# Kernel tuning notes

Hardware: AMD Instinct MI355X
Metric: run time of the kernel (lower is better)

The kernel has to match this reference:

```python
import jax, jax.numpy as jnp
import numpy as np

# --- configuration (matches init_kwargs) ---
K = 8            # number of cluster fields
L = 8            # hashgrid levels
T = 2 ** 18      # hash table size per level (log2_hashmap_size=18)
F = 2            # features per level
HID = 64         # MLP hidden dim
BASE_RES = 16    # base resolution; max_res=2048 -> growth factor 2
N_PTS = 524288

PRIMES = np.array([1, 2654435761, 805459861], dtype=np.uint32)
RES = (BASE_RES * 2 ** np.arange(L)).astype(np.float32)  # [16,32,...,2048]
CORNERS = np.array([[i, j, k] for i in (0, 1) for j in (0, 1) for k in (0, 1)],
                   dtype=np.float32)  # [8,3] trilinear corner offsets


def setup_inputs() -> dict:
    key = jax.random.key(0)
    ks = jax.random.split(key, 6)
    return {
        "positions": jax.random.uniform(ks[0], (N_PTS, 3), dtype=jnp.float32),
        "centroids": jax.random.uniform(ks[1], (K, 3), dtype=jnp.float32),
        "tables":    jax.random.normal(ks[2], (K, L, T, F), dtype=jnp.float32) * 1e-2,
        "W1":        jax.random.normal(ks[3], (K, L * F, HID), dtype=jnp.float32) * 0.1,
        "b1":        jnp.zeros((K, HID), dtype=jnp.float32),
        "W2":        jax.random.normal(ks[4], (K, HID, 1), dtype=jnp.float32) * 0.1,
        "b2":        jnp.zeros((K, 1), dtype=jnp.float32),
    }


def _hash_encode(positions, tables, assign):
    """Multi-resolution hash encoding, table selected per-point by cluster assignment."""
    N = positions.shape[0]
    res = jnp.asarray(RES)                                    # [L]
    scaled = positions[:, None, :] * res[None, :, None]       # [N,L,3]
    f = jnp.floor(scaled)
    w = scaled - f                                            # [N,L,3] trilinear fracs
    corners = jnp.asarray(CORNERS)                            # [8,3]
    ci = (f[:, :, None, :] + corners[None, None]).astype(jnp.uint32)  # [N,L,8,3]
    p = jnp.asarray(PRIMES)
    h = (ci[..., 0] * p[0]) ^ (ci[..., 1] * p[1]) ^ (ci[..., 2] * p[2])
    h = (h & jnp.uint32(T - 1)).astype(jnp.int32)             # [N,L,8]
    lvl = jnp.arange(L, dtype=jnp.int32)
    # flat index into [K*L*T, F] table selects the assigned field's grid
    flat = (assign[:, None, None] * L + lvl[None, :, None]) * T + h   # [N,L,8]
    feats = tables.reshape(K * L * T, F)[flat]                # [N,L,8,F] gather
    cw = jnp.prod(jnp.where(corners[None, None] > 0.5,
                            w[:, :, None, :], 1.0 - w[:, :, None, :]), axis=-1)  # [N,L,8]
    enc = jnp.sum(feats * cw[..., None], axis=2)              # [N,L,F]
    return enc.reshape(N, L * F)


def reference(positions, centroids, tables, W1, b1, W2, b2):
    # cdist + argmin cluster routing
    d2 = jnp.sum((positions[:, None, :] - centroids[None]) ** 2, axis=-1)  # [N,K]
    assign = jnp.argmin(d2, axis=1).astype(jnp.int32)                      # [N]
    enc = _hash_encode(positions, tables, assign)                          # [N, L*F]
    dens = jnp.zeros((positions.shape[0], 1), dtype=positions.dtype)
    for k in range(K):  # small fixed loop over structurally distinct fields
        h = jax.nn.relu(enc @ W1[k] + b1[k])
        dk = jnp.exp(h @ W2[k] + b2[k])  # trunc_exp density activation
        dens = jnp.where((assign == k)[:, None], dk, dens)
    return dens  # [N,1]
```

## Files before the change

kernel.cpp:

```cpp
#include <hip/hip_runtime.h>
#include <hip/hip_fp16.h>
#include <math.h>

#define KF 8
#define LL 8
#define TT (1 << 18)
#define FF 2
#define HID 64
#define INF 16
#define W1S 1056
#define BS  68

#define NENT (KF * LL * TT)
#define TAB_BYTES ((size_t)NENT * 4)


__global__ __launch_bounds__(256) void repack_tables_fp16(
    const float4* __restrict__ src, uint4* __restrict__ dst, int nthreads)
{
    const int gid = blockIdx.x * blockDim.x + threadIdx.x;
    if (gid >= nthreads) return;
    const size_t b = (size_t)gid * 4;

    const float4 f0 = src[b + 0];
    const float4 f1 = src[b + 1];
    const float4 f2 = src[b + 2];
    const float4 f3 = src[b + 3];

    uint4 d0, d1;
    {
        __half2 h;
        h = __floats2half2_rn(f0.x, f0.y); d0.x = *reinterpret_cast<unsigned*>(&h);
        h = __floats2half2_rn(f0.z, f0.w); d0.y = *reinterpret_cast<unsigned*>(&h);
        h = __floats2half2_rn(f1.x, f1.y); d0.z = *reinterpret_cast<unsigned*>(&h);
        h = __floats2half2_rn(f1.z, f1.w); d0.w = *reinterpret_cast<unsigned*>(&h);
        h = __floats2half2_rn(f2.x, f2.y); d1.x = *reinterpret_cast<unsigned*>(&h);
        h = __floats2half2_rn(f2.z, f2.w); d1.y = *reinterpret_cast<unsigned*>(&h);
        h = __floats2half2_rn(f3.x, f3.y); d1.z = *reinterpret_cast<unsigned*>(&h);
        h = __floats2half2_rn(f3.z, f3.w); d1.w = *reinterpret_cast<unsigned*>(&h);
    }
    dst[(size_t)gid * 2 + 0] = d0;
    dst[(size_t)gid * 2 + 1] = d1;
}

__global__ void zero_cursors(unsigned* __restrict__ cursors)
{
    if (threadIdx.x < KF) cursors[threadIdx.x] = 0u;
}

__global__ __launch_bounds__(256) void bucket_points(
    const float* __restrict__ positions,
    const float* __restrict__ centroids,
    unsigned* __restrict__ cursors,
    unsigned* __restrict__ indices,
    int npts)
{
    __shared__ float sC[KF * 3];
    __shared__ unsigned lcnt[KF];
    __shared__ unsigned lbase[KF];

    const int tid = threadIdx.x;
    if (tid < KF * 3) sC[tid] = centroids[tid];
    if (tid < KF) lcnt[tid] = 0u;
    __syncthreads();

    const int gid = blockIdx.x * blockDim.x + tid;
    int assign = 0;
    unsigned lrank = 0;
    const bool valid = (gid < npts);
    if (valid) {
        const float px = positions[gid * 3 + 0];
        const float py = positions[gid * 3 + 1];
        const float pz = positions[gid * 3 + 2];
        float best = 1e30f;
        #pragma unroll
        for (int k = 0; k < KF; ++k) {
            float dx = px - sC[k * 3 + 0];
            float dy = py - sC[k * 3 + 1];
            float dz = pz - sC[k * 3 + 2];
            float d2 = fmaf(dx, dx, fmaf(dy, dy, dz * dz));
            bool lt = d2 < best;
            assign = lt ? k : assign;
            best = lt ? d2 : best;
        }
        lrank = atomicAdd(&lcnt[assign], 1u);
    }
    __syncthreads();
    if (tid < KF) lbase[tid] = atomicAdd(&cursors[tid], lcnt[tid]);
    __syncthreads();
    if (valid)
        indices[(size_t)assign * npts + lbase[assign] + lrank] = (unsigned)gid;
}

__global__ __launch_bounds__(256) void propnet_density_balanced(
    const float* __restrict__ positions,
    const __half2* __restrict__ tables,
    const float* __restrict__ W1,
    const float* __restrict__ b1,
    const float* __restrict__ W2,
    const float* __restrict__ b2,
    const unsigned* __restrict__ cursors,
    const unsigned* __restrict__ indices,
    float* __restrict__ out,
    int npts, int cpx)
{
    __shared__ float sW1[INF * HID];
    __shared__ float sB1[HID];
    __shared__ float sW2[HID];
    __shared__ unsigned snk[KF];

    const int tid = threadIdx.x;
    const int b = blockIdx.x;
    const int v = (b & 7) * cpx + (b >> 3);

    if (tid < KF) snk[tid] = cursors[tid];
    __syncthreads();

    int k = -1;
    unsigned slot = 0, nk = 0, acc = 0;
    #pragma unroll
    for (int kk = 0; kk < KF; ++kk) {
        const unsigned n = snk[kk];
        const unsigned nbk = (n + 255u) >> 8;
        if (k < 0 && (unsigned)v < acc + nbk) {
            k = kk; slot = (unsigned)v - acc; nk = n;
        }
        acc += nbk;
    }
    if (k < 0) return;

    for (int idx = tid; idx < INF * HID; idx += blockDim.x)
        sW1[idx] = W1[k * (INF * HID) + idx];
    if (tid < HID) {
        sB1[tid] = b1[k * HID + tid];
        sW2[tid] = W2[k * HID + tid];
    }
    __syncthreads();

    const unsigned rank = slot * 256u + (unsigned)tid;
    if (rank >= nk) return;
    const unsigned pidx = indices[(size_t)k * npts + rank];

    const float px = positions[pidx * 3 + 0];
    const float py = positions[pidx * 3 + 1];
    const float pz = positions[pidx * 3 + 2];

    float enc[INF];
    const __half2* __restrict__ tab = tables + (size_t)k * (LL * (size_t)TT);

    #pragma unroll
    for (int l = 0; l < LL; ++l) {
        const float res = (float)(16 << l);
        const float sx = px * res, sy = py * res, sz = pz * res;
        const float fx = floorf(sx), fy = floorf(sy), fz = floorf(sz);
        const float wx = sx - fx, wy = sy - fy, wz = sz - fz;
        const unsigned ix = (unsigned)(int)fx;
        const unsigned iy = (unsigned)(int)fy;
        const unsigned iz = (unsigned)(int)fz;

        const __half2* __restrict__ tl = tab + (size_t)l * TT;

        const unsigned hx0 = ix;
        const unsigned hx1 = ix + 1u;
        const unsigned hy0 = iy * 2654435761u;
        const unsigned hy1 = (iy + 1u) * 2654435761u;
        const unsigned hz0 = iz * 805459861u;
        const unsigned hz1 = (iz + 1u) * 805459861u;
        const unsigned M = TT - 1;

        const __half2 c000 = tl[(hx0 ^ hy0 ^ hz0) & M];
        const __half2 c001 = tl[(hx0 ^ hy0 ^ hz1) & M];
        const __half2 c010 = tl[(hx0 ^ hy1 ^ hz0) & M];
        const __half2 c011 = tl[(hx0 ^ hy1 ^ hz1) & M];
        const __half2 c100 = tl[(hx1 ^ hy0 ^ hz0) & M];
        const __half2 c101 = tl[(hx1 ^ hy0 ^ hz1) & M];
        const __half2 c110 = tl[(hx1 ^ hy1 ^ hz0) & M];
        const __half2 c111 = tl[(hx1 ^ hy1 ^ hz1) & M];

        const float ux = 1.f - wx, uy = 1.f - wy, uz = 1.f - wz;
        const float w000 = ux * uy * uz, w001 = ux * uy * wz;
        const float w010 = ux * wy * uz, w011 = ux * wy * wz;
        const float w100 = wx * uy * uz, w101 = wx * uy * wz;
        const float w110 = wx * wy * uz, w111 = wx * wy * wz;

        enc[l * 2 + 0] = __low2float(c000) * w000 + __low2float(c001) * w001
                       + __low2float(c010) * w010 + __low2float(c011) * w011
                       + __low2float(c100) * w100 + __low2float(c101) * w101
                       + __low2float(c110) * w110 + __low2float(c111) * w111;
        enc[l * 2 + 1] = __high2float(c000) * w000 + __high2float(c001) * w001
                       + __high2float(c010) * w010 + __high2float(c011) * w011
                       + __high2float(c100) * w100 + __high2float(c101) * w101
                       + __high2float(c110) * w110 + __high2float(c111) * w111;
    }

    const float4* __restrict__ w1k = (const float4*)sW1;
    const float4* __restrict__ b1k = (const float4*)sB1;
    const float4* __restrict__ w2k = (const float4*)sW2;

    float outv = b2[k];
    #pragma unroll
    for (int j4 = 0; j4 < HID / 4; ++j4) {
        float4 a = b1k[j4];
        #pragma unroll
        for (int i = 0; i < INF; ++i) {
            const float4 w = w1k[i * (HID / 4) + j4];
            const float e = enc[i];
            a.x = fmaf(e, w.x, a.x);
            a.y = fmaf(e, w.y, a.y);
            a.z = fmaf(e, w.z, a.z);
            a.w = fmaf(e, w.w, a.w);
        }
        a.x = fmaxf(a.x, 0.f); a.y = fmaxf(a.y, 0.f);
        a.z = fmaxf(a.z, 0.f); a.w = fmaxf(a.w, 0.f);
        const float4 w2v = w2k[j4];
        outv = fmaf(a.x, w2v.x, outv);
        outv = fmaf(a.y, w2v.y, outv);
        outv = fmaf(a.z, w2v.z, outv);
        outv = fmaf(a.w, w2v.w, outv);
    }

    out[pidx] = expf(outv);
}

__global__ __launch_bounds__(256) void propnet_density_kernel_h(
    const float* __restrict__ positions,
    const float* __restrict__ centroids,
    const __half2* __restrict__ tables,
    const float* __restrict__ W1,
    const float* __restrict__ b1,
    const float* __restrict__ W2,
    const float* __restrict__ b2,
    float* __restrict__ out,
    int npts)
{
    __shared__ float sW1[KF * W1S];
    __shared__ float sB1[KF * BS];
    __shared__ float sW2[KF * BS];
    __shared__ float sB2[KF];
    __shared__ float sC[KF * 3];

    const int tid = threadIdx.x;

    for (int idx = tid; idx < KF * INF * HID; idx += blockDim.x) {
        int k = idx >> 10;
        int r = idx & 1023;
        sW1[k * W1S + r] = W1[idx];
    }
    for (int idx = tid; idx < KF * HID; idx += blockDim.x) {
        int k = idx >> 6;
        int r = idx & 63;
        sB1[k * BS + r] = b1[idx];
        sW2[k * BS + r] = W2[idx];
    }
    if (tid < KF) sB2[tid] = b2[tid];
    if (tid < KF * 3) sC[tid] = centroids[tid];
    __syncthreads();

    const int gid = blockIdx.x * blockDim.x + tid;
    if (gid >= npts) return;

    const float px = positions[gid * 3 + 0];
    const float py = positions[gid * 3 + 1];
    const float pz = positions[gid * 3 + 2];

    int assign = 0;
    float best = 1e30f;
    #pragma unroll
    for (int k = 0; k < KF; ++k) {
        float dx = px - sC[k * 3 + 0];
        float dy = py - sC[k * 3 + 1];
        float dz = pz - sC[k * 3 + 2];
        float d2 = fmaf(dx, dx, fmaf(dy, dy, dz * dz));
        bool lt = d2 < best;
        assign = lt ? k : assign;
        best = lt ? d2 : best;
    }

    float enc[INF];
    const __half2* __restrict__ tab =
        tables + (size_t)assign * (LL * (size_t)TT);

    #pragma unroll
    for (int l = 0; l < LL; ++l) {
        const float res = (float)(16 << l);
        const float sx = px * res, sy = py * res, sz = pz * res;
        const float fx = floorf(sx), fy = floorf(sy), fz = floorf(sz);
        const float wx = sx - fx, wy = sy - fy, wz = sz - fz;
        const unsigned ix = (unsigned)(int)fx;
        const unsigned iy = (unsigned)(int)fy;
        const unsigned iz = (unsigned)(int)fz;

        const __half2* __restrict__ tl = tab + (size_t)l * TT;

        const unsigned hx0 = ix;
        const unsigned hx1 = ix + 1u;
        const unsigned hy0 = iy * 2654435761u;
        const unsigned hy1 = (iy + 1u) * 2654435761u;
        const unsigned hz0 = iz * 805459861u;
        const unsigned hz1 = (iz + 1u) * 805459861u;
        const unsigned M = TT - 1;

        const __half2 c000 = tl[(hx0 ^ hy0 ^ hz0) & M];
        const __half2 c001 = tl[(hx0 ^ hy0 ^ hz1) & M];
        const __half2 c010 = tl[(hx0 ^ hy1 ^ hz0) & M];
        const __half2 c011 = tl[(hx0 ^ hy1 ^ hz1) & M];
        const __half2 c100 = tl[(hx1 ^ hy0 ^ hz0) & M];
        const __half2 c101 = tl[(hx1 ^ hy0 ^ hz1) & M];
        const __half2 c110 = tl[(hx1 ^ hy1 ^ hz0) & M];
        const __half2 c111 = tl[(hx1 ^ hy1 ^ hz1) & M];

        const float ux = 1.f - wx, uy = 1.f - wy, uz = 1.f - wz;
        const float w000 = ux * uy * uz, w001 = ux * uy * wz;
        const float w010 = ux * wy * uz, w011 = ux * wy * wz;
        const float w100 = wx * uy * uz, w101 = wx * uy * wz;
        const float w110 = wx * wy * uz, w111 = wx * wy * wz;

        enc[l * 2 + 0] = __low2float(c000) * w000 + __low2float(c001) * w001
                       + __low2float(c010) * w010 + __low2float(c011) * w011
                       + __low2float(c100) * w100 + __low2float(c101) * w101
                       + __low2float(c110) * w110 + __low2float(c111) * w111;
        enc[l * 2 + 1] = __high2float(c000) * w000 + __high2float(c001) * w001
                       + __high2float(c010) * w010 + __high2float(c011) * w011
                       + __high2float(c100) * w100 + __high2float(c101) * w101
                       + __high2float(c110) * w110 + __high2float(c111) * w111;
    }

    const float4* __restrict__ w1k = (const float4*)(sW1 + assign * W1S);
    const float4* __restrict__ b1k = (const float4*)(sB1 + assign * BS);
    const float4* __restrict__ w2k = (const float4*)(sW2 + assign * BS);

    float outv = sB2[assign];
    #pragma unroll
    for (int j4 = 0; j4 < HID / 4; ++j4) {
        float4 a = b1k[j4];
        #pragma unroll
        for (int i = 0; i < INF; ++i) {
            const float4 w = w1k[i * (HID / 4) + j4];
            const float e = enc[i];
            a.x = fmaf(e, w.x, a.x);
            a.y = fmaf(e, w.y, a.y);
            a.z = fmaf(e, w.z, a.z);
            a.w = fmaf(e, w.w, a.w);
        }
        a.x = fmaxf(a.x, 0.f); a.y = fmaxf(a.y, 0.f);
        a.z = fmaxf(a.z, 0.f); a.w = fmaxf(a.w, 0.f);
        const float4 w2v = w2k[j4];
        outv = fmaf(a.x, w2v.x, outv);
        outv = fmaf(a.y, w2v.y, outv);
        outv = fmaf(a.z, w2v.z, outv);
        outv = fmaf(a.w, w2v.w, outv);
    }

    out[gid] = expf(outv);
}

__global__ __launch_bounds__(256) void propnet_density_kernel_f(
    const float* __restrict__ positions,
    const float* __restrict__ centroids,
    const float* __restrict__ tables,
    const float* __restrict__ W1,
    const float* __restrict__ b1,
    const float* __restrict__ W2,
    const float* __restrict__ b2,
    float* __restrict__ out,
    int npts)
{
    __shared__ float sW1[KF * W1S];
    __shared__ float sB1[KF * BS];
    __shared__ float sW2[KF * BS];
    __shared__ float sB2[KF];
    __shared__ float sC[KF * 3];

    const int tid = threadIdx.x;

    for (int idx = tid; idx < KF * INF * HID; idx += blockDim.x) {
        int k = idx >> 10;
        int r = idx & 1023;
        sW1[k * W1S + r] = W1[idx];
    }
    for (int idx = tid; idx < KF * HID; idx += blockDim.x) {
        int k = idx >> 6;
        int r = idx & 63;
        sB1[k * BS + r] = b1[idx];
        sW2[k * BS + r] = W2[idx];
    }
    if (tid < KF) sB2[tid] = b2[tid];
    if (tid < KF * 3) sC[tid] = centroids[tid];
    __syncthreads();

    const int gid = blockIdx.x * blockDim.x + tid;
    if (gid >= npts) return;

    const float px = positions[gid * 3 + 0];
    const float py = positions[gid * 3 + 1];
    const float pz = positions[gid * 3 + 2];

    int assign = 0;
    float best = 1e30f;
    #pragma unroll
    for (int k = 0; k < KF; ++k) {
        float dx = px - sC[k * 3 + 0];
        float dy = py - sC[k * 3 + 1];
        float dz = pz - sC[k * 3 + 2];
        float d2 = fmaf(dx, dx, fmaf(dy, dy, dz * dz));
        bool lt = d2 < best;
        assign = lt ? k : assign;
        best = lt ? d2 : best;
    }

    float enc[INF];
    const float2* __restrict__ tab =
        (const float2*)tables + (size_t)assign * (LL * (size_t)TT);

    #pragma unroll
    for (int l = 0; l < LL; ++l) {
        const float res = (float)(16 << l);
        const float sx = px * res, sy = py * res, sz = pz * res;
        const float fx = floorf(sx), fy = floorf(sy), fz = floorf(sz);
        const float wx = sx - fx, wy = sy - fy, wz = sz - fz;
        const unsigned ix = (unsigned)(int)fx;
        const unsigned iy = (unsigned)(int)fy;
        const unsigned iz = (unsigned)(int)fz;

        const float2* __restrict__ tl = tab + (size_t)l * TT;

        const unsigned hx0 = ix;
        const unsigned hx1 = ix + 1u;
        const unsigned hy0 = iy * 2654435761u;
        const unsigned hy1 = (iy + 1u) * 2654435761u;
        const unsigned hz0 = iz * 805459861u;
        const unsigned hz1 = (iz + 1u) * 805459861u;
        const unsigned M = TT - 1;

        const float2 c000 = tl[(hx0 ^ hy0 ^ hz0) & M];
        const float2 c001 = tl[(hx0 ^ hy0 ^ hz1) & M];
        const float2 c010 = tl[(hx0 ^ hy1 ^ hz0) & M];
        const float2 c011 = tl[(hx0 ^ hy1 ^ hz1) & M];
        const float2 c100 = tl[(hx1 ^ hy0 ^ hz0) & M];
        const float2 c101 = tl[(hx1 ^ hy0 ^ hz1) & M];
        const float2 c110 = tl[(hx1 ^ hy1 ^ hz0) & M];
        const float2 c111 = tl[(hx1 ^ hy1 ^ hz1) & M];

        const float ux = 1.f - wx, uy = 1.f - wy, uz = 1.f - wz;
        const float w000 = ux * uy * uz, w001 = ux * uy * wz;
        const float w010 = ux * wy * uz, w011 = ux * wy * wz;
        const float w100 = wx * uy * uz, w101 = wx * uy * wz;
        const float w110 = wx * wy * uz, w111 = wx * wy * wz;

        enc[l * 2 + 0] = c000.x * w000 + c001.x * w001 + c010.x * w010 + c011.x * w011
                       + c100.x * w100 + c101.x * w101 + c110.x * w110 + c111.x * w111;
        enc[l * 2 + 1] = c000.y * w000 + c001.y * w001 + c010.y * w010 + c011.y * w011
                       + c100.y * w100 + c101.y * w101 + c110.y * w110 + c111.y * w111;
    }

    const float4* __restrict__ w1k = (const float4*)(sW1 + assign * W1S);
    const float4* __restrict__ b1k = (const float4*)(sB1 + assign * BS);
    const float4* __restrict__ w2k = (const float4*)(sW2 + assign * BS);

    float outv = sB2[assign];
    #pragma unroll
    for (int j4 = 0; j4 < HID / 4; ++j4) {
        float4 a = b1k[j4];
        #pragma unroll
        for (int i = 0; i < INF; ++i) {
            const float4 w = w1k[i * (HID / 4) + j4];
            const float e = enc[i];
            a.x = fmaf(e, w.x, a.x);
            a.y = fmaf(e, w.y, a.y);
            a.z = fmaf(e, w.z, a.z);
            a.w = fmaf(e, w.w, a.w);
        }
        a.x = fmaxf(a.x, 0.f); a.y = fmaxf(a.y, 0.f);
        a.z = fmaxf(a.z, 0.f); a.w = fmaxf(a.w, 0.f);
        const float4 w2v = w2k[j4];
        outv = fmaf(a.x, w2v.x, outv);
        outv = fmaf(a.y, w2v.y, outv);
        outv = fmaf(a.z, w2v.z, outv);
        outv = fmaf(a.w, w2v.w, outv);
    }

    out[gid] = expf(outv);
}

extern "C" void kernel_launch(void* const* d_in, const int* in_sizes, int n_in,
                              void* d_out, int out_size, void* d_ws, size_t ws_size,
                              hipStream_t stream) {
    const float* positions = (const float*)d_in[0];
    const float* centroids = (const float*)d_in[1];
    const float* tables    = (const float*)d_in[2];
    const float* W1        = (const float*)d_in[3];
    const float* b1        = (const float*)d_in[4];
    const float* W2        = (const float*)d_in[5];
    const float* b2        = (const float*)d_in[6];
    float* out = (float*)d_out;

    const int npts = in_sizes[0] / 3;
    const int block = 256;
    const int nb = (npts + block - 1) / block;

    const size_t need_h    = TAB_BYTES;
    const size_t need_full = TAB_BYTES + 256 + (size_t)KF * npts * 4;

    if (ws_size >= need_full && d_ws != nullptr) {
        char* base = (char*)d_ws;
        __half2*  wsTab   = (__half2*)base;
        unsigned* cursors = (unsigned*)(base + TAB_BYTES);
        unsigned* indices = (unsigned*)(base + TAB_BYTES + 256);

        const int rthreads = NENT / 8;
        repack_tables_fp16<<<rthreads / 256, 256, 0, stream>>>(
            (const float4*)tables, (uint4*)wsTab, rthreads);
        zero_cursors<<<1, 64, 0, stream>>>(cursors);
        bucket_points<<<nb, block, 0, stream>>>(
            positions, centroids, cursors, indices, npts);

        const int G = ((nb + KF + 7) / 8) * 8;
        const int cpx = G / 8;
        propnet_density_balanced<<<G, block, 0, stream>>>(
            positions, wsTab, W1, b1, W2, b2, cursors, indices, out, npts, cpx);
    } else if (ws_size >= need_h && d_ws != nullptr) {
        const int rthreads = NENT / 8;
        repack_tables_fp16<<<rthreads / 256, 256, 0, stream>>>(
            (const float4*)tables, (uint4*)d_ws, rthreads);
        propnet_density_kernel_h<<<nb, block, 0, stream>>>(
            positions, centroids, (const __half2*)d_ws, W1, b1, W2, b2, out, npts);
    } else {
        propnet_density_kernel_f<<<nb, block, 0, stream>>>(
            positions, centroids, tables, W1, b1, W2, b2, out, npts);
    }
}
```

Measured before the change: 366.8 us.

## Sort points by cluster and coarse spatial cell before hash-grid evaluation

Replaces the per-cluster bucketing with a counting sort keyed on (cluster, 16^3 spatial cell). A histogram pass, a single-block scan and a scatter pass order the point indices so that neighbouring threads query nearby hash-table entries, which should improve cache locality of the random gathers. This adds three extra kernel launches and a second pass over the positions, plus global atomics on 32K counters. The order of points within a cell is nondeterministic.

```diff
diff --git a/kernel.cpp b/kernel.cpp
--- a/kernel.cpp
+++ b/kernel.cpp
@@ -13,6 +13,9 @@
 
 #define NENT (KF * LL * TT)
 #define TAB_BYTES ((size_t)NENT * 4)
+
+#define NCELL 4096
+#define NKEY  (KF * NCELL)
 
 
 __global__ __launch_bounds__(256) void repack_tables_fp16(
@@ -43,6 +46,118 @@
     dst[(size_t)gid * 2 + 1] = d1;
 }
 
+
+__device__ __forceinline__ int argmin_cluster(
+    const float* sC, float px, float py, float pz)
+{
+    int assign = 0;
+    float best = 1e30f;
+    #pragma unroll
+    for (int k = 0; k < KF; ++k) {
+        float dx = px - sC[k * 3 + 0];
+        float dy = py - sC[k * 3 + 1];
+        float dz = pz - sC[k * 3 + 2];
+        float d2 = fmaf(dx, dx, fmaf(dy, dy, dz * dz));
+        bool lt = d2 < best;
+        assign = lt ? k : assign;
+        best = lt ? d2 : best;
+    }
+    return assign;
+}
+
+__device__ __forceinline__ unsigned cell16(float px, float py, float pz)
+{
+    int cx = (int)(px * 16.f); cx = cx < 0 ? 0 : (cx > 15 ? 15 : cx);
+    int cy = (int)(py * 16.f); cy = cy < 0 ? 0 : (cy > 15 ? 15 : cy);
+    int cz = (int)(pz * 16.f); cz = cz < 0 ? 0 : (cz > 15 ? 15 : cz);
+    return (unsigned)(cx + cy * 16 + cz * 256);
+}
+
+__global__ __launch_bounds__(256) void zero_hist(unsigned* __restrict__ hist)
+{
+    const int gid = blockIdx.x * blockDim.x + threadIdx.x;
+    if (gid < NKEY) hist[gid] = 0u;
+}
+
+__global__ __launch_bounds__(256) void assign_hist(
+    const float* __restrict__ positions,
+    const float* __restrict__ centroids,
+    unsigned* __restrict__ hist, int npts)
+{
+    __shared__ float sC[KF * 3];
+    const int tid = threadIdx.x;
+    if (tid < KF * 3) sC[tid] = centroids[tid];
+    __syncthreads();
+
+    const int gid = blockIdx.x * blockDim.x + tid;
+    if (gid >= npts) return;
+    const float px = positions[gid * 3 + 0];
+    const float py = positions[gid * 3 + 1];
+    const float pz = positions[gid * 3 + 2];
+    const int k = argmin_cluster(sC, px, py, pz);
+    const unsigned key = (unsigned)k * NCELL + cell16(px, py, pz);
+    atomicAdd(&hist[key], 1u);
+}
+
+__global__ __launch_bounds__(1024) void scan_hist(
+    unsigned* __restrict__ hist, unsigned* __restrict__ cursors, int npts)
+{
+    __shared__ unsigned s[1024];
+    __shared__ unsigned cs[KF];
+    const int t = threadIdx.x;
+    const int base = t * (NKEY / 1024);
+
+    unsigned loc[NKEY / 1024];
+    unsigned sum = 0;
+    #pragma unroll
+    for (int i = 0; i < NKEY / 1024; ++i) { loc[i] = hist[base + i]; sum += loc[i]; }
+    s[t] = sum;
+    __syncthreads();
+
+    for (int off = 1; off < 1024; off <<= 1) {
+        unsigned v = (t >= off) ? s[t - off] : 0u;
+        __syncthreads();
+        s[t] += v;
+        __syncthreads();
+    }
+    const unsigned excl = s[t] - sum;
+
+    unsigned run = excl;
+    #pragma unroll
+    for (int i = 0; i < NKEY / 1024; ++i) { hist[base + i] = run; run += loc[i]; }
+
+    if ((t & 127) == 0 && (t >> 7) < KF) cs[t >> 7] = excl;
+    __syncthreads();
+    if (t < KF) {
+        cursors[8 + t] = cs[t];
+        cursors[t] = ((t == KF - 1) ? (unsigned)npts : cs[t + 1]) - cs[t];
+    }
+}
+
+__global__ __launch_bounds__(256) void scatter_sorted(
+    const float* __restrict__ positions,
+    const float* __restrict__ centroids,
+    unsigned* __restrict__ hist,
+    const unsigned* __restrict__ cursors,
+    unsigned* __restrict__ indices, int npts)
+{
+    __shared__ float sC[KF * 3];
+    const int tid = threadIdx.x;
+    if (tid < KF * 3) sC[tid] = centroids[tid];
+    __syncthreads();
+
+    const int gid = blockIdx.x * blockDim.x + tid;
+    if (gid >= npts) return;
+    const float px = positions[gid * 3 + 0];
+    const float py = positions[gid * 3 + 1];
+    const float pz = positions[gid * 3 + 2];
+    const int k = argmin_cluster(sC, px, py, pz);
+    const unsigned key = (unsigned)k * NCELL + cell16(px, py, pz);
+    const unsigned pos = atomicAdd(&hist[key], 1u);
+    const unsigned rank = pos - cursors[8 + k];
+    indices[(size_t)k * npts + rank] = (unsigned)gid;
+}
+
 __global__ void zero_cursors(unsigned* __restrict__ cursors)
 {
     if (threadIdx.x < KF) cursors[threadIdx.x] = 0u;
@@ -72,17 +187,7 @@
         const float px = positions[gid * 3 + 0];
         const float py = positions[gid * 3 + 1];
         const float pz = positions[gid * 3 + 2];
-        float best = 1e30f;
-        #pragma unroll
-        for (int k = 0; k < KF; ++k) {
-            float dx = px - sC[k * 3 + 0];
-            float dy = py - sC[k * 3 + 1];
-            float dz = pz - sC[k * 3 + 2];
-            float d2 = fmaf(dx, dx, fmaf(dy, dy, dz * dz));
-            bool lt = d2 < best;
-            assign = lt ? k : assign;
-            best = lt ? d2 : best;
-        }
+        assign = argmin_cluster(sC, px, py, pz);
         lrank = atomicAdd(&lcnt[assign], 1u);
     }
     __syncthreads();
@@ -263,18 +368,7 @@
     const float py = positions[gid * 3 + 1];
     const float pz = positions[gid * 3 + 2];
 
-    int assign = 0;
-    float best = 1e30f;
-    #pragma unroll
-    for (int k = 0; k < KF; ++k) {
-        float dx = px - sC[k * 3 + 0];
-        float dy = py - sC[k * 3 + 1];
-        float dz = pz - sC[k * 3 + 2];
-        float d2 = fmaf(dx, dx, fmaf(dy, dy, dz * dz));
-        bool lt = d2 < best;
-        assign = lt ? k : assign;
-        best = lt ? d2 : best;
-    }
+    int assign = argmin_cluster(sC, px, py, pz);
 
     float enc[INF];
     const __half2* __restrict__ tab =
@@ -395,18 +489,7 @@
     const float py = positions[gid * 3 + 1];
     const float pz = positions[gid * 3 + 2];
 
-    int assign = 0;
-    float best = 1e30f;
-    #pragma unroll
-    for (int k = 0; k < KF; ++k) {
-        float dx = px - sC[k * 3 + 0];
-        float dy = py - sC[k * 3 + 1];
-        float dz = pz - sC[k * 3 + 2];
-        float d2 = fmaf(dx, dx, fmaf(dy, dy, dz * dz));
-        bool lt = d2 < best;
-        assign = lt ? k : assign;
-        best = lt ? d2 : best;
-    }
+    int assign = argmin_cluster(sC, px, py, pz);
 
     float enc[INF];
     const float2* __restrict__ tab =
@@ -498,10 +581,12 @@
     const int block = 256;
     const int nb = (npts + block - 1) / block;
 
-    const size_t need_h    = TAB_BYTES;
-    const size_t need_full = TAB_BYTES + 256 + (size_t)KF * npts * 4;
-
-    if (ws_size >= need_full && d_ws != nullptr) {
+    const size_t idx_bytes   = (size_t)KF * npts * 4;
+    const size_t need_h      = TAB_BYTES;
+    const size_t need_bucket = TAB_BYTES + 256 + idx_bytes;
+    const size_t need_sorted = need_bucket + (size_t)NKEY * 4;
+
+    if (ws_size >= need_bucket && d_ws != nullptr) {
         char* base = (char*)d_ws;
         __half2*  wsTab   = (__half2*)base;
         unsigned* cursors = (unsigned*)(base + TAB_BYTES);
@@ -510,9 +595,19 @@
         const int rthreads = NENT / 8;
         repack_tables_fp16<<<rthreads / 256, 256, 0, stream>>>(
             (const float4*)tables, (uint4*)wsTab, rthreads);
-        zero_cursors<<<1, 64, 0, stream>>>(cursors);
-        bucket_points<<<nb, block, 0, stream>>>(
-            positions, centroids, cursors, indices, npts);
+
+        if (ws_size >= need_sorted) {
+            unsigned* hist = (unsigned*)(base + TAB_BYTES + 256 + idx_bytes);
+            zero_hist<<<NKEY / 256, 256, 0, stream>>>(hist);
+            assign_hist<<<nb, block, 0, stream>>>(positions, centroids, hist, npts);
+            scan_hist<<<1, 1024, 0, stream>>>(hist, cursors, npts);
+            scatter_sorted<<<nb, block, 0, stream>>>(
+                positions, centroids, hist, cursors, indices, npts);
+        } else {
+            zero_cursors<<<1, 64, 0, stream>>>(cursors);
+            bucket_points<<<nb, block, 0, stream>>>(
+                positions, centroids, cursors, indices, npts);
+        }
 
         const int G = ((nb + KF + 7) / 8) * 8;
         const int cpx = G / 8;
```

New measurement: 444.5 us. 1.21x slower.
